# Optimization experiments

Hardware: AMD Instinct MI355X
Metric: run time of the kernel (lower is better)

Reference implementation:

```python
import jax, jax.numpy as jnp
import numpy as np

H = 1024  # hidden_dim

def setup_inputs() -> dict:
    key = jax.random.key(0)
    ks = jax.random.split(key, 6)
    B, T, D = 4096, 28, 28
    x = jax.random.normal(ks[0], (B, T, D), dtype=jnp.float32)
    key_seq = jax.random.normal(ks[1], (8, T, D), dtype=jnp.float32)
    s_ih = 1.0 / np.sqrt(D)
    s_hh = 1.0 / np.sqrt(H)
    W_ih = jax.random.normal(ks[2], (D, 4 * H), dtype=jnp.float32) * s_ih
    W_hh = jax.random.normal(ks[3], (H, 4 * H), dtype=jnp.float32) * s_hh
    b = jnp.zeros((4 * H,), dtype=jnp.float32)
    W_cls = jax.random.normal(ks[4], (H, 10), dtype=jnp.float32) * s_hh
    b_cls = jnp.zeros((10,), dtype=jnp.float32)
    return {"x": x, "key_seq": key_seq, "W_ih": W_ih, "W_hh": W_hh,
            "b": b, "W_cls": W_cls, "b_cls": b_cls}


def _lstm_last(xs, h0, c0, W_ih, W_hh, b):
    """Run LSTM over xs [B,T,D]; return final (h, c), each [B,H]."""
    xs_t = jnp.swapaxes(xs, 0, 1)  # [T,B,D]

    def step(carry, xt):
        h, c = carry
        g = xt @ W_ih + h @ W_hh + b  # [B,4H]
        i, f, gg, o = jnp.split(g, 4, axis=-1)
        c = jax.nn.sigmoid(f) * c + jax.nn.sigmoid(i) * jnp.tanh(gg)
        h = jax.nn.sigmoid(o) * jnp.tanh(c)
        return (h, c), None

    (h, c), _ = jax.lax.scan(step, (h0, c0), xs_t)
    return h, c


def reference(x, key_seq, W_ih, W_hh, b, W_cls, b_cls):
    B = x.shape[0]
    Kb = key_seq.shape[0]
    zk = jnp.zeros((Kb, H), dtype=x.dtype)
    # key modulation: run the key sequences through the same recurrence;
    # the mean final state seeds the initial state for the data pass.
    hk, ck = _lstm_last(key_seq, zk, zk, W_ih, W_hh, b)
    h0 = jnp.broadcast_to(hk.mean(axis=0), (B, H))
    c0 = jnp.broadcast_to(ck.mean(axis=0), (B, H))
    h, _ = _lstm_last(x, h0, c0, W_ih, W_hh, b)
    # dropout is identity in eval mode
    return h @ W_cls + b_cls  # [B,10]
```

## Files before the change

### kernel.cpp

```cpp
#include <hip/hip_runtime.h>
#include <hip/hip_bf16.h>
#include <stdint.h>

#define HID 1024
#define G4H 4096
#define BATCH 4096
#define TSTEPS 28
#define DIN 28
#define KTOT 1056
#define NKEY 8
#define NTILES 33

typedef __attribute__((ext_vector_type(8))) __bf16 b16x8;
typedef __attribute__((ext_vector_type(4))) __bf16 b16x4;
typedef __attribute__((ext_vector_type(4))) float f32x4;
typedef __attribute__((address_space(1))) unsigned int u32_g;
typedef __attribute__((address_space(3))) unsigned int u32_l;

__device__ __forceinline__ void async16(const __hip_bfloat16* g, __hip_bfloat16* l) {
  __builtin_amdgcn_global_load_lds((u32_g*)g, (u32_l*)l, 16, 0, 0);
}

__device__ __forceinline__ float sigmoidf_(float x) { return 1.f / (1.f + __expf(-x)); }
__device__ __forceinline__ float tanhfast_(float x) { return 2.f / (1.f + __expf(-2.f * x)) - 1.f; }

__device__ __forceinline__ int nprime(int gate, int j) {
  return ((j >> 4) << 6) + (gate << 4) + (j & 15);
}

__global__ __launch_bounds__(256) void prep_weights(
    const float* __restrict__ W_hh, const float* __restrict__ W_ih,
    __hip_bfloat16* __restrict__ Wt, float* __restrict__ kstate) {
  __shared__ float tile[64][65];
  const int k0 = blockIdx.x * 64, n0 = blockIdx.y * 64;
  const int tid = threadIdx.x;
  const int fid = (blockIdx.y * gridDim.x + blockIdx.x) * 256 + tid;
  if (fid < 2 * NKEY * HID) kstate[fid] = 0.f;
  for (int i = tid; i < 4096; i += 256) {
    int kk = i >> 6, nn = i & 63;
    int k = k0 + kk;
    float v = 0.f;
    if (k < HID) v = W_hh[k * G4H + n0 + nn];
    else if (k < HID + DIN) v = W_ih[(k - HID) * G4H + n0 + nn];
    tile[kk][nn] = v;
  }
  __syncthreads();
  for (int i = tid; i < 4096; i += 256) {
    int nn = i >> 6, kk = i & 63;
    int k = k0 + kk;
    int n = n0 + nn;
    int np = nprime(n >> 10, n & 1023);
    if (k < KTOT) Wt[(size_t)np * KTOT + k] = __float2bfloat16(tile[kk][nn]);
  }
}

__global__ __launch_bounds__(256) void key_step(
    const __hip_bfloat16* __restrict__ Wt, const float* __restrict__ key_seq,
    const float* __restrict__ bias, const float* __restrict__ hk_in,
    float* __restrict__ hk_out, float* __restrict__ ck, int t) {
  __shared__ float sh[NKEY][KTOT];
  __shared__ float sred[32][8][8];
  const int tid = threadIdx.x;
#pragma unroll
  for (int key = 0; key < NKEY; ++key)
    for (int k = tid; k < HID; k += 256) sh[key][k] = hk_in[key * HID + k];
  for (int i = tid; i < NKEY * 32; i += 256) {
    int key = i >> 5, d = i & 31;
    sh[key][HID + d] = (d < DIN) ? key_seq[key * (TSTEPS * DIN) + t * DIN + d] : 0.f;
  }
  __syncthreads();
  const int rowIdx = tid >> 3;
  const int kpart = tid & 7;
  const int gate = rowIdx >> 3, jj = rowIdx & 7;
  const int j0 = blockIdx.x * 8;
  const int np = nprime(gate, j0 + jj);
  const __hip_bfloat16* wrow = Wt + (size_t)np * KTOT + kpart * 132;
  const int kb = kpart * 132;
  float acc[NKEY];
#pragma unroll
  for (int key = 0; key < NKEY; ++key) acc[key] = 0.f;
  for (int kk = 0; kk < 132; kk += 4) {
    b16x4 wv = *(const b16x4*)(wrow + kk);
    float w0 = (float)wv[0], w1 = (float)wv[1], w2 = (float)wv[2], w3 = (float)wv[3];
#pragma unroll
    for (int key = 0; key < NKEY; ++key) {
      const float* s = &sh[key][kb + kk];
      acc[key] += w0 * s[0] + w1 * s[1] + w2 * s[2] + w3 * s[3];
    }
  }
#pragma unroll
  for (int key = 0; key < NKEY; ++key) sred[rowIdx][kpart][key] = acc[key];
  __syncthreads();
  if (tid < 64) {
    int key = tid >> 3, j2 = tid & 7;
    float g[4];
#pragma unroll
    for (int gg = 0; gg < 4; ++gg) {
      float s = 0.f;
#pragma unroll
      for (int p = 0; p < 8; ++p) s += sred[gg * 8 + j2][p][key];
      g[gg] = s + bias[gg * HID + j0 + j2];
    }
    size_t ci = (size_t)key * HID + j0 + j2;
    float cv = sigmoidf_(g[1]) * ck[ci] + sigmoidf_(g[0]) * tanhfast_(g[2]);
    ck[ci] = cv;
    hk_out[ci] = sigmoidf_(g[3]) * tanhfast_(cv);
  }
}

__global__ __launch_bounds__(256) void key_mean(
    const float* __restrict__ hk, const float* __restrict__ ck,
    float* __restrict__ h0, float* __restrict__ c0) {
  int j = blockIdx.x * 256 + threadIdx.x;
  float sh_ = 0.f, sc_ = 0.f;
#pragma unroll
  for (int k = 0; k < NKEY; ++k) { sh_ += hk[k * HID + j]; sc_ += ck[k * HID + j]; }
  h0[j] = sh_ * (1.f / NKEY);
  c0[j] = sc_ * (1.f / NKEY);
}

__global__ __launch_bounds__(256) void main_init(
    const float* __restrict__ h0, const float* __restrict__ c0,
    const float* __restrict__ x, __hip_bfloat16* __restrict__ A0,
    __hip_bfloat16* __restrict__ A1, float* __restrict__ c) {
  int idx = blockIdx.x * 256 + threadIdx.x;
  int b = idx / KTOT, col = idx - b * KTOT;
  if (col < HID) {
    A0[idx] = __float2bfloat16(h0[col]);
    c[b * HID + col] = c0[col];
  } else if (col < HID + DIN) {
    A0[idx] = __float2bfloat16(x[b * (TSTEPS * DIN) + (col - HID)]);
  } else {
    A0[idx] = __float2bfloat16(0.f);
    A1[idx] = __float2bfloat16(0.f);
  }
}

__global__ __launch_bounds__(512, 4) void gemm_lstm(
    const __hip_bfloat16* __restrict__ Ain, const __hip_bfloat16* __restrict__ Wt,
    const float* __restrict__ bias, float* __restrict__ cst,
    __hip_bfloat16* __restrict__ Aout, const float* __restrict__ x,
    float* __restrict__ hfin, int t) {
  __shared__ alignas(16) __hip_bfloat16 sA[2][256 * 32];
  __shared__ alignas(16) __hip_bfloat16 sB[2][4 * 32 * 32];
  const int tid = threadIdx.x;
  const int lane = tid & 63, wave = tid >> 6;
  const int wr = wave >> 1, wc = wave & 1;
  const int jt = blockIdx.x, mt = blockIdx.y;
  const int brow = mt * 256, j0 = jt * 32;
  const int lrow = lane & 15, kq = lane >> 4;
  const int sx = (lrow >> 1) & 3;

  const int kqs = (tid & 3) ^ ((tid >> 3) & 3);
  const int sArow = tid >> 2;
  const int sBr = tid >> 2;
  const __hip_bfloat16* gA0 = Ain + (size_t)(brow + sArow) * KTOT + kqs * 8;
  const __hip_bfloat16* gA1 = gA0 + (size_t)128 * KTOT;
  const __hip_bfloat16* gB = Wt + (size_t)nprime(sBr >> 5, j0 + (sBr & 31)) * KTOT + kqs * 8;

  int iA[4];
#pragma unroll
  for (int m = 0; m < 4; ++m) {
    int row = wr * 64 + m * 16 + lrow;
    iA[m] = row * 4 + (kq ^ sx);
  }
  int iB[4];
  {
    int jl = wc * 16 + lrow;
#pragma unroll
    for (int g = 0; g < 4; ++g) iB[g] = (g * 32 + jl) * 4 + (kq ^ sx);
  }

  f32x4 acc[4][4] = {};

#define STAGE(buf, kt) do { \
    async16(gA0 + (size_t)(kt) * 32, &sA[buf][tid * 8]); \
    async16(gA1 + (size_t)(kt) * 32, &sA[buf][4096 + tid * 8]); \
    async16(gB + (size_t)(kt) * 32, &sB[buf][tid * 8]); \
  } while (0)

  STAGE(0, 0);
  __syncthreads();

  for (int kt = 0; kt < NTILES; ++kt) {
    if (kt + 1 < NTILES) STAGE((kt + 1) & 1, kt + 1);
    const b16x8* cA = (const b16x8*)sA[kt & 1];
    const b16x8* cB = (const b16x8*)sB[kt & 1];
    b16x8 af[4], bf[4];
#pragma unroll
    for (int m = 0; m < 4; ++m) af[m] = cA[iA[m]];
#pragma unroll
    for (int g = 0; g < 4; ++g) bf[g] = cB[iB[g]];
    __builtin_amdgcn_s_setprio(1);
#pragma unroll
    for (int g = 0; g < 4; ++g)
#pragma unroll
      for (int m = 0; m < 4; ++m)
        acc[g][m] = __builtin_amdgcn_mfma_f32_16x16x32_bf16(af[m], bf[g], acc[g][m], 0, 0, 0);
    __builtin_amdgcn_s_setprio(0);
    __syncthreads();
  }
#undef STAGE

  const int j = j0 + wc * 16 + lrow;
  const float b_i = bias[j], b_f = bias[HID + j];
  const float b_g = bias[2 * HID + j], b_o = bias[3 * HID + j];
#pragma unroll
  for (int m = 0; m < 4; ++m) {
    const int row0 = brow + wr * 64 + m * 16 + kq * 4;
#pragma unroll
    for (int r = 0; r < 4; ++r) {
      const int row = row0 + r;
      const size_t ci = (size_t)row * HID + j;
      float gi = acc[0][m][r] + b_i;
      float gf = acc[1][m][r] + b_f;
      float gg = acc[2][m][r] + b_g;
      float go = acc[3][m][r] + b_o;
      float cv = sigmoidf_(gf) * cst[ci] + sigmoidf_(gi) * tanhfast_(gg);
      cst[ci] = cv;
      float h = sigmoidf_(go) * tanhfast_(cv);
      Aout[(size_t)row * KTOT + j] = __float2bfloat16(h);
      if (t == TSTEPS - 1) hfin[ci] = h;
    }
  }
  if (jt == 0 && t + 1 < TSTEPS) {
    for (int i = tid; i < 256 * DIN; i += 512) {
      int rr = i / DIN, d = i - rr * DIN;
      Aout[(size_t)(brow + rr) * KTOT + HID + d] =
          __float2bfloat16(x[(size_t)(brow + rr) * (TSTEPS * DIN) + (t + 1) * DIN + d]);
    }
  }
}

__global__ __launch_bounds__(256) void classifier(
    const float* __restrict__ hfin, const float* __restrict__ W_cls,
    const float* __restrict__ b_cls, float* __restrict__ out) {
  __shared__ float sw[HID * 10];
  __shared__ float sred[10][257];
  const int b = blockIdx.x, tid = threadIdx.x;
  for (int i = tid; i < HID * 10; i += 256) sw[i] = W_cls[i];
  __syncthreads();
  float acc[10];
#pragma unroll
  for (int cls = 0; cls < 10; ++cls) acc[cls] = 0.f;
  for (int j = tid; j < HID; j += 256) {
    float hv = hfin[(size_t)b * HID + j];
#pragma unroll
    for (int cls = 0; cls < 10; ++cls) acc[cls] += hv * sw[j * 10 + cls];
  }
#pragma unroll
  for (int cls = 0; cls < 10; ++cls) sred[cls][tid] = acc[cls];
  __syncthreads();
  for (int off = 128; off > 0; off >>= 1) {
    if (tid < off)
#pragma unroll
      for (int cls = 0; cls < 10; ++cls) sred[cls][tid] += sred[cls][tid + off];
    __syncthreads();
  }
  if (tid < 10) out[b * 10 + tid] = sred[tid][0] + b_cls[tid];
}

extern "C" void kernel_launch(void* const* d_in, const int* in_sizes, int n_in,
                              void* d_out, int out_size, void* d_ws, size_t ws_size,
                              hipStream_t stream) {
  const float* x      = (const float*)d_in[0];
  const float* keyseq = (const float*)d_in[1];
  const float* W_ih   = (const float*)d_in[2];
  const float* W_hh   = (const float*)d_in[3];
  const float* bias   = (const float*)d_in[4];
  const float* W_cls  = (const float*)d_in[5];
  const float* b_cls  = (const float*)d_in[6];
  float* out = (float*)d_out;
  (void)in_sizes; (void)n_in; (void)out_size; (void)ws_size;

  char* p = (char*)d_ws;
  auto alloc = [&](size_t bytes) { char* r = p; p += (bytes + 255) & ~(size_t)255; return r; };
  __hip_bfloat16* Wt = (__hip_bfloat16*)alloc((size_t)G4H * KTOT * 2);
  __hip_bfloat16* A0 = (__hip_bfloat16*)alloc((size_t)BATCH * KTOT * 2);
  __hip_bfloat16* A1 = (__hip_bfloat16*)alloc((size_t)BATCH * KTOT * 2);
  float* c    = (float*)alloc((size_t)BATCH * HID * 4);
  float* hfin = (float*)alloc((size_t)BATCH * HID * 4);
  float* hk0  = (float*)alloc((size_t)NKEY * HID * 4);
  float* ck   = (float*)alloc((size_t)NKEY * HID * 4);
  float* hk1  = (float*)alloc((size_t)NKEY * HID * 4);
  float* h0   = (float*)alloc((size_t)HID * 4);
  float* c0   = (float*)alloc((size_t)HID * 4);

  prep_weights<<<dim3(17, 64), 256, 0, stream>>>(W_hh, W_ih, Wt, hk0);

  float* kbuf[2] = {hk0, hk1};
  for (int t = 0; t < TSTEPS; ++t)
    key_step<<<128, 256, 0, stream>>>(Wt, keyseq, bias, kbuf[t & 1], kbuf[(t + 1) & 1], ck, t);
  key_mean<<<4, 256, 0, stream>>>(hk0, ck, h0, c0);

  main_init<<<(BATCH * KTOT) / 256, 256, 0, stream>>>(h0, c0, x, A0, A1, c);

  __hip_bfloat16* Ab[2] = {A0, A1};
  for (int t = 0; t < TSTEPS; ++t)
    gemm_lstm<<<dim3(32, 16), 512, 0, stream>>>(Ab[t & 1], Wt, bias, c,
                                                Ab[(t + 1) & 1], x, hfin, t);
  classifier<<<BATCH, 256, 0, stream>>>(hfin, W_cls, b_cls, out);
}
```

Baseline: 2.022 ms.

## Triple-buffer GEMM K-loop, transpose cell state, stage h stores through LDS

The gemm_lstm K-loop moves from double to triple buffering with a prefetch distance of two. It uses explicit vmcnt waits and raw barriers in place of __syncthreads, so loads overlap further with MFMA work. The cell state is stored transposed as [H][B], which lets each thread load and store its c values as contiguous float4 vectors held in registers, prefetched before the loop. The h output is written to LDS first and then stored to global memory as 16-byte vectors instead of scattered 2-byte stores. The cost is more LDS per block, which may reduce occupancy, plus a new c_init kernel launch.

```diff
diff --git a/kernel.cpp b/kernel.cpp
--- a/kernel.cpp
+++ b/kernel.cpp
@@ -120,14 +120,12 @@
 }
 
 __global__ __launch_bounds__(256) void main_init(
-    const float* __restrict__ h0, const float* __restrict__ c0,
-    const float* __restrict__ x, __hip_bfloat16* __restrict__ A0,
-    __hip_bfloat16* __restrict__ A1, float* __restrict__ c) {
+    const float* __restrict__ h0, const float* __restrict__ x,
+    __hip_bfloat16* __restrict__ A0, __hip_bfloat16* __restrict__ A1) {
   int idx = blockIdx.x * 256 + threadIdx.x;
   int b = idx / KTOT, col = idx - b * KTOT;
   if (col < HID) {
     A0[idx] = __float2bfloat16(h0[col]);
-    c[b * HID + col] = c0[col];
   } else if (col < HID + DIN) {
     A0[idx] = __float2bfloat16(x[b * (TSTEPS * DIN) + (col - HID)]);
   } else {
@@ -136,13 +134,21 @@
   }
 }
 
+__global__ __launch_bounds__(256) void c_init(
+    const float* __restrict__ c0, float* __restrict__ cT) {
+  int i4 = blockIdx.x * 256 + threadIdx.x;
+  float v = c0[i4 >> 10];
+  float4 w = {v, v, v, v};
+  ((float4*)cT)[i4] = w;
+}
+
 __global__ __launch_bounds__(512, 4) void gemm_lstm(
     const __hip_bfloat16* __restrict__ Ain, const __hip_bfloat16* __restrict__ Wt,
     const float* __restrict__ bias, float* __restrict__ cst,
     __hip_bfloat16* __restrict__ Aout, const float* __restrict__ x,
     float* __restrict__ hfin, int t) {
-  __shared__ alignas(16) __hip_bfloat16 sA[2][256 * 32];
-  __shared__ alignas(16) __hip_bfloat16 sB[2][4 * 32 * 32];
+  __shared__ alignas(16) __hip_bfloat16 sA[3][256 * 32];
+  __shared__ alignas(16) __hip_bfloat16 sB[3][4 * 32 * 32];
   const int tid = threadIdx.x;
   const int lane = tid & 63, wave = tid >> 6;
   const int wr = wave >> 1, wc = wave & 1;
@@ -171,6 +177,14 @@
     for (int g = 0; g < 4; ++g) iB[g] = (g * 32 + jl) * 4 + (kq ^ sx);
   }
 
+  const int j = j0 + wc * 16 + lrow;
+  float* cbase = cst + (size_t)j * BATCH + brow + wr * 64 + kq * 4;
+  f32x4 creg[4];
+#pragma unroll
+  for (int m = 0; m < 4; ++m) creg[m] = *(const f32x4*)(cbase + m * 16);
+  const float b_i = bias[j], b_f = bias[HID + j];
+  const float b_g = bias[2 * HID + j], b_o = bias[3 * HID + j];
+
   f32x4 acc[4][4] = {};
 
 #define STAGE(buf, kt) do { \
@@ -180,12 +194,16 @@
   } while (0)
 
   STAGE(0, 0);
-  __syncthreads();
-
+  STAGE(1, 1);
+  asm volatile("s_waitcnt vmcnt(3)" ::: "memory");
+  __builtin_amdgcn_s_barrier();
+
+#pragma unroll 3
   for (int kt = 0; kt < NTILES; ++kt) {
-    if (kt + 1 < NTILES) STAGE((kt + 1) & 1, kt + 1);
-    const b16x8* cA = (const b16x8*)sA[kt & 1];
-    const b16x8* cB = (const b16x8*)sB[kt & 1];
+    const int cb = kt % 3;
+    if (kt + 2 < NTILES) STAGE((kt + 2) % 3, kt + 2);
+    const b16x8* cA = (const b16x8*)sA[cb];
+    const b16x8* cB = (const b16x8*)sB[cb];
     b16x8 af[4], bf[4];
 #pragma unroll
     for (int m = 0; m < 4; ++m) af[m] = cA[iA[m]];
@@ -198,30 +216,40 @@
       for (int m = 0; m < 4; ++m)
         acc[g][m] = __builtin_amdgcn_mfma_f32_16x16x32_bf16(af[m], bf[g], acc[g][m], 0, 0, 0);
     __builtin_amdgcn_s_setprio(0);
-    __syncthreads();
+    if (kt + 2 < NTILES)      asm volatile("s_waitcnt vmcnt(3)" ::: "memory");
+    else if (kt + 1 < NTILES) asm volatile("s_waitcnt vmcnt(0)" ::: "memory");
+    __builtin_amdgcn_s_barrier();
   }
 #undef STAGE
 
-  const int j = j0 + wc * 16 + lrow;
-  const float b_i = bias[j], b_f = bias[HID + j];
-  const float b_g = bias[2 * HID + j], b_o = bias[3 * HID + j];
+  __hip_bfloat16* sH = &sA[0][0];
 #pragma unroll
   for (int m = 0; m < 4; ++m) {
-    const int row0 = brow + wr * 64 + m * 16 + kq * 4;
+    f32x4 cv4 = creg[m];
 #pragma unroll
     for (int r = 0; r < 4; ++r) {
-      const int row = row0 + r;
-      const size_t ci = (size_t)row * HID + j;
       float gi = acc[0][m][r] + b_i;
       float gf = acc[1][m][r] + b_f;
       float gg = acc[2][m][r] + b_g;
       float go = acc[3][m][r] + b_o;
-      float cv = sigmoidf_(gf) * cst[ci] + sigmoidf_(gi) * tanhfast_(gg);
-      cst[ci] = cv;
+      float cv = sigmoidf_(gf) * cv4[r] + sigmoidf_(gi) * tanhfast_(gg);
+      cv4[r] = cv;
       float h = sigmoidf_(go) * tanhfast_(cv);
-      Aout[(size_t)row * KTOT + j] = __float2bfloat16(h);
-      if (t == TSTEPS - 1) hfin[ci] = h;
+      const int lr = wr * 64 + m * 16 + kq * 4 + r;
+      sH[lr * 32 + wc * 16 + lrow] = __float2bfloat16(h);
+      if (t == TSTEPS - 1) hfin[(size_t)(brow + lr) * HID + j] = h;
     }
+    *(f32x4*)(cbase + m * 16) = cv4;
+  }
+  __syncthreads();
+  {
+    const b16x8* sHv = (const b16x8*)sH;
+    const int lr = tid >> 1, seg = tid & 1;
+    __hip_bfloat16* dst = Aout + (size_t)(brow + lr) * KTOT + j0 + seg * 16;
+    b16x8 v0 = sHv[lr * 4 + seg * 2];
+    b16x8 v1 = sHv[lr * 4 + seg * 2 + 1];
+    *(b16x8*)dst = v0;
+    *(b16x8*)(dst + 8) = v1;
   }
   if (jt == 0 && t + 1 < TSTEPS) {
     for (int i = tid; i < 256 * DIN; i += 512) {
@@ -278,7 +306,7 @@
   __hip_bfloat16* Wt = (__hip_bfloat16*)alloc((size_t)G4H * KTOT * 2);
   __hip_bfloat16* A0 = (__hip_bfloat16*)alloc((size_t)BATCH * KTOT * 2);
   __hip_bfloat16* A1 = (__hip_bfloat16*)alloc((size_t)BATCH * KTOT * 2);
-  float* c    = (float*)alloc((size_t)BATCH * HID * 4);
+  float* cT   = (float*)alloc((size_t)BATCH * HID * 4);
   float* hfin = (float*)alloc((size_t)BATCH * HID * 4);
   float* hk0  = (float*)alloc((size_t)NKEY * HID * 4);
   float* ck   = (float*)alloc((size_t)NKEY * HID * 4);
@@ -293,11 +321,12 @@
     key_step<<<128, 256, 0, stream>>>(Wt, keyseq, bias, kbuf[t & 1], kbuf[(t + 1) & 1], ck, t);
   key_mean<<<4, 256, 0, stream>>>(hk0, ck, h0, c0);
 
-  main_init<<<(BATCH * KTOT) / 256, 256, 0, stream>>>(h0, c0, x, A0, A1, c);
+  main_init<<<(BATCH * KTOT) / 256, 256, 0, stream>>>(h0, x, A0, A1);
+  c_init<<<(BATCH * HID / 4) / 256, 256, 0, stream>>>(c0, cT);
 
   __hip_bfloat16* Ab[2] = {A0, A1};
   for (int t = 0; t < TSTEPS; ++t)
-    gemm_lstm<<<dim3(32, 16), 512, 0, stream>>>(Ab[t & 1], Wt, bias, c,
+    gemm_lstm<<<dim3(32, 16), 512, 0, stream>>>(Ab[t & 1], Wt, bias, cT,
                                                 Ab[(t + 1) & 1], x, hfin, t);
   classifier<<<BATCH, 256, 0, stream>>>(hfin, W_cls, b_cls, out);
 }
```

Result: slower. 2.920 ms (+44.4%).
